# Optimization experiments

Measured on AMD Instinct MI355X. Metric: run time of the kernel, lower is better.

The kernel has to match this reference:

```python
import jax, jax.numpy as jnp
import numpy as np

D_MODEL = 1024
SEL_DIM = 64
CONFIGS = [(4, 32), (8, 64), (16, 128)]  # (heads, dim)
B, T = 2, 2048


def setup_inputs() -> dict:
    key = jax.random.key(0)
    ks = jax.random.split(key, 20)
    s = 0.02  # init scale for stability
    inp = {
        "x": jax.random.normal(ks[0], (B, T, D_MODEL), jnp.float32),
        "sel_w1": jax.random.normal(ks[1], (SEL_DIM, D_MODEL), jnp.float32) * s,
        "sel_b1": jnp.zeros((SEL_DIM,), jnp.float32),
        "sel_w2": jax.random.normal(ks[2], (SEL_DIM, SEL_DIM), jnp.float32) * s,
        "sel_b2": jnp.zeros((SEL_DIM,), jnp.float32),
        "sel_w3": jax.random.normal(ks[3], (len(CONFIGS), SEL_DIM), jnp.float32) * s,
        "sel_b3": jnp.zeros((len(CONFIGS),), jnp.float32),
    }
    for i, (h, d) in enumerate(CONFIGS):
        inp[f"qw{i}"] = jax.random.normal(ks[4 + 3 * i], (h * d, D_MODEL), jnp.float32) * s
        inp[f"kw{i}"] = jax.random.normal(ks[5 + 3 * i], (d, D_MODEL), jnp.float32) * s
        inp[f"ww{i}"] = jax.random.normal(ks[6 + 3 * i], (h, D_MODEL), jnp.float32) * s
    return inp


def _seq_features(x):
    # x: [b,t,d]
    b, t, d = x.shape
    seq_mean = jnp.mean(x, axis=1, keepdims=True)            # [b,1,d]
    seq_std = jnp.std(x, axis=1, keepdims=True, ddof=1)      # torch.std is unbiased
    pos = (jnp.arange(t, dtype=x.dtype) / t)[None, :, None]  # [1,t,1] broadcast to [b,t,d]
    return x + seq_mean + seq_std + pos * 0.1


def _forward(x, sel_w1, sel_b1, sel_w2, sel_b2, sel_w3, sel_b3,
             qw0, kw0, ww0, qw1, kw1, ww1, qw2, kw2, ww2):
    b, t, dm = x.shape
    feats = _seq_features(x)
    h1 = jax.nn.relu(feats @ sel_w1.T + sel_b1)
    h2 = jax.nn.relu(h1 @ sel_w2.T + sel_b2)
    config_probs = jax.nn.softmax(h2 @ sel_w3.T + sel_b3, axis=-1)  # [b,t,ncfg]

    per_cfg = [(qw0, kw0, ww0), (qw1, kw1, ww1), (qw2, kw2, ww2)]
    final = jnp.zeros((b, t, t), dtype=x.dtype)
    for i, ((heads, dim), (qw, kw, ww)) in enumerate(zip(CONFIGS, per_cfg)):
        q = (x @ qw.T).reshape(b, t, heads, dim)   # [b,t,h,d]
        k = x @ kw.T                               # [b,s,d]
        w = x @ ww.T                               # [b,t,h]
        dots = jnp.einsum('bthd,bsd->bths', q, k)  # [b,t,h,s]
        score = jnp.einsum('bths,bth->bts', jax.nn.relu(dots), w)  # relu*weight, sum heads
        final = final + config_probs[:, :, i:i + 1] * score
    return final


def reference(x, sel_w1, sel_b1, sel_w2, sel_b2, sel_w3, sel_b3,
              qw0, kw0, ww0, qw1, kw1, ww1, qw2, kw2, ww2):
    return _forward(x, sel_w1, sel_b1, sel_w2, sel_b2, sel_w3, sel_b3,
                    qw0, kw0, ww0, qw1, kw1, ww1, qw2, kw2, ww2)
```

## Files before the change

kernel.cpp:

```cpp
#include <hip/hip_runtime.h>
#include <cstdint>
#include <cstddef>
#include <math.h>

#define B_ 2
#define T_ 2048
#define D_ 1024
#define M_ (B_*T_)

#define QO0 0
#define KO0 128
#define WO0 160
#define QO1 168
#define KO1 680
#define WO1 744
#define QO2 752
#define KO2 2800
#define WO2 2928
#define SELO 2944
#define LDN 3072

typedef float f32x16 __attribute__((ext_vector_type(16)));
typedef short bf16x8 __attribute__((ext_vector_type(8)));
typedef unsigned short u16;

__device__ __forceinline__ u16 f2bf(float f) {
    unsigned int u = __float_as_uint(f);
    unsigned int r = (u + 0x7fffu + ((u >> 16) & 1u)) >> 16;
    return (u16)r;
}
__device__ __forceinline__ float bf2f(u16 b) {
    return __uint_as_float(((unsigned int)b) << 16);
}

__device__ __forceinline__ void gload16(const void* g, void* l) {
    __builtin_amdgcn_global_load_lds(
        (const __attribute__((address_space(1))) unsigned int*)g,
        (__attribute__((address_space(3))) unsigned int*)l,
        16, 0, 0);
}

__device__ __forceinline__ void stage_plane(const u16* src_base, int row_stride, int k0,
                                            int rg, int lane, u16* dst) {
    int rl  = lane >> 2;
    int row = rg * 16 + rl;
    int q   = (lane & 3) ^ (rl & 3) ^ ((rl >> 2) & 3);
    const u16* s = src_base + (size_t)row * row_stride + k0 + q * 8;
    gload16(s, dst + rg * 512);
}

__global__ void stats_partial(const float* __restrict__ x,
                              float* __restrict__ part, float* __restrict__ part2) {
    int d  = blockIdx.x * 256 + threadIdx.x;
    int tc = blockIdx.y;
    int b  = blockIdx.z;
    const float* p = x + (size_t)b * T_ * D_ + (size_t)tc * 128 * D_ + d;
    float s = 0.f, s2 = 0.f;
    for (int t = 0; t < 128; ++t) {
        float v = p[(size_t)t * D_];
        s += v; s2 += v * v;
    }
    part [(b * 16 + tc) * D_ + d] = s;
    part2[(b * 16 + tc) * D_ + d] = s2;
}

__global__ void stats_final(const float* __restrict__ part, const float* __restrict__ part2,
                            float* __restrict__ ms) {
    int idx = blockIdx.x * 256 + threadIdx.x;
    if (idx >= B_ * D_) return;
    int b = idx / D_, d = idx % D_;
    float s = 0.f, s2 = 0.f;
    for (int i = 0; i < 16; ++i) {
        s  += part [(b * 16 + i) * D_ + d];
        s2 += part2[(b * 16 + i) * D_ + d];
    }
    float mean = s / (float)T_;
    float var  = (s2 - (float)T_ * mean * mean) / (float)(T_ - 1);
    ms[idx] = mean + sqrtf(fmaxf(var, 0.f));
}

__global__ void msdot(const float* __restrict__ ms, const float* __restrict__ w1,
                      float* __restrict__ msd, float* __restrict__ s1) {
    int b = blockIdx.x, j = threadIdx.x;
    const float* wr = w1 + (size_t)j * D_;
    const float* mr = ms + (size_t)b * D_;
    float am = 0.f, as = 0.f;
    for (int d4 = 0; d4 < D_ / 4; ++d4) {
        float4 w = *(const float4*)(wr + d4 * 4);
        float4 m = *(const float4*)(mr + d4 * 4);
        am += w.x * m.x + w.y * m.y + w.z * m.z + w.w * m.w;
        as += w.x + w.y + w.z + w.w;
    }
    msd[b * 64 + j] = am;
    if (b == 0) s1[j] = as;
}

__global__ void split_w(const float* __restrict__ qw0, const float* __restrict__ kw0,
                        const float* __restrict__ ww0, const float* __restrict__ qw1,
                        const float* __restrict__ kw1, const float* __restrict__ ww1,
                        const float* __restrict__ qw2, const float* __restrict__ kw2,
                        const float* __restrict__ ww2, const float* __restrict__ w1s,
                        u16* __restrict__ Wh) {
    int row = blockIdx.x;
    int col = threadIdx.x * 4;
    const float* src = nullptr;
    if      (row < 128)  src = qw0 + (size_t)row * D_;
    else if (row < 160)  src = kw0 + (size_t)(row - 128) * D_;
    else if (row < 164)  src = ww0 + (size_t)(row - 160) * D_;
    else if (row < 168)  src = nullptr;
    else if (row < 680)  src = qw1 + (size_t)(row - 168) * D_;
    else if (row < 744)  src = kw1 + (size_t)(row - 680) * D_;
    else if (row < 752)  src = ww1 + (size_t)(row - 744) * D_;
    else if (row < 2800) src = qw2 + (size_t)(row - 752) * D_;
    else if (row < 2928) src = kw2 + (size_t)(row - 2800) * D_;
    else if (row < 2944) src = ww2 + (size_t)(row - 2928) * D_;
    else if (row < 3008) src = w1s + (size_t)(row - 2944) * D_;
    float4 v = src ? *(const float4*)(src + col) : make_float4(0.f, 0.f, 0.f, 0.f);
    ushort4 h;
    h.x = f2bf(v.x); h.y = f2bf(v.y); h.z = f2bf(v.z); h.w = f2bf(v.w);
    *(ushort4*)&Wh[(size_t)row * D_ + col] = h;
}

__global__ void cast_x(const float* __restrict__ x, u16* __restrict__ Xh) {
    size_t i = ((size_t)blockIdx.x * 256 + threadIdx.x) * 4;
    float4 v = *(const float4*)(x + i);
    ushort4 h;
    h.x = f2bf(v.x); h.y = f2bf(v.y); h.z = f2bf(v.z); h.w = f2bf(v.w);
    *(ushort4*)&Xh[i] = h;
}

__global__ __launch_bounds__(256, 4) void proj_gemm(
    const u16* __restrict__ Xh, const u16* __restrict__ Wh, u16* __restrict__ Ph) {
    __shared__ u16 As[2][4096], Bs[2][4096];
    int tid = threadIdx.x;
    int wave = tid >> 6, lane = tid & 63;
    int bm = blockIdx.x * 128, bn = blockIdx.y * 128;
    int wt = wave >> 1, wn = wave & 1;
    int fm = lane & 31, hv = lane >> 5;
    int tkey = (fm & 3) ^ ((fm >> 2) & 3);
    f32x16 acc[2][2];
#pragma unroll
    for (int i = 0; i < 2; ++i)
#pragma unroll
        for (int j = 0; j < 2; ++j)
#pragma unroll
            for (int r = 0; r < 16; ++r) acc[i][j][r] = 0.f;

    const u16* xh = Xh + (size_t)bm * D_;
    const u16* wh = Wh + (size_t)bn * D_;

    auto stage = [&](int buf, int k0) {
#pragma unroll
        for (int i = 0; i < 4; ++i) {
            int j = wave * 4 + i;
            int pl = j >> 3, rg = j & 7;
            stage_plane(pl ? wh : xh, D_, k0, rg, lane, pl ? Bs[buf] : As[buf]);
        }
    };

    stage(0, 0);
    for (int kc = 0; kc < 32; ++kc) {
        __syncthreads();
        if (kc + 1 < 32) stage((kc + 1) & 1, (kc + 1) * 32);
        const u16* ah = As[kc & 1];
        const u16* bh = Bs[kc & 1];
#pragma unroll
        for (int ks = 0; ks < 2; ++ks) {
            int slot8 = ((ks * 2 + hv) ^ tkey) * 8;
            bf16x8 a_h[2], b_h[2];
#pragma unroll
            for (int t = 0; t < 2; ++t) {
                a_h[t] = *(const bf16x8*)&ah[(wt * 64 + t * 32 + fm) * 32 + slot8];
                b_h[t] = *(const bf16x8*)&bh[(wn * 64 + t * 32 + fm) * 32 + slot8];
            }
#pragma unroll
            for (int ti = 0; ti < 2; ++ti)
#pragma unroll
                for (int tj = 0; tj < 2; ++tj)
                    acc[ti][tj] = __builtin_amdgcn_mfma_f32_32x32x16_bf16(a_h[ti], b_h[tj], acc[ti][tj], 0, 0, 0);
        }
    }
#pragma unroll
    for (int ti = 0; ti < 2; ++ti)
#pragma unroll
        for (int tj = 0; tj < 2; ++tj)
#pragma unroll
            for (int r = 0; r < 16; ++r) {
                int row = bm + wt * 64 + ti * 32 + (r & 3) + 8 * (r >> 2) + 4 * (lane >> 5);
                int col = bn + wn * 64 + tj * 32 + (lane & 31);
                Ph[(size_t)row * LDN + col] = f2bf(acc[ti][tj][r]);
            }
}

__global__ void selector2(const u16* __restrict__ Ph,
                          const float* __restrict__ msd, const float* __restrict__ s1,
                          const float* __restrict__ b1, const float* __restrict__ w2,
                          const float* __restrict__ b2, const float* __restrict__ w3,
                          const float* __restrict__ b3, float* __restrict__ PR) {
    __shared__ float h1s[4][64];
    __shared__ float h2s[4][64];
    __shared__ float lg[4][3];
    int tid = threadIdx.x;
    int slot = tid >> 6, j = tid & 63;
    int bt = blockIdx.x * 4 + slot;
    int b = bt >> 11, t = bt & 2047;
    size_t pidx = (size_t)bt * LDN + SELO + j;
    float v = bf2f(Ph[pidx])
            + msd[b * 64 + j] + 0.1f * ((float)t / (float)T_) * s1[j] + b1[j];
    h1s[slot][j] = fmaxf(v, 0.f);
    __syncthreads();
    float a2 = b2[j];
#pragma unroll 8
    for (int d = 0; d < 64; ++d) a2 = fmaf(h1s[slot][d], w2[j * 64 + d], a2);
    h2s[slot][j] = fmaxf(a2, 0.f);
    __syncthreads();
    if (j < 3) {
        float a3 = b3[j];
        for (int d = 0; d < 64; ++d) a3 = fmaf(h2s[slot][d], w3[j * 64 + d], a3);
        lg[slot][j] = a3;
    }
    __syncthreads();
    if (j == 0) {
        float m = fmaxf(lg[slot][0], fmaxf(lg[slot][1], lg[slot][2]));
        float e0 = expf(lg[slot][0] - m), e1 = expf(lg[slot][1] - m), e2 = expf(lg[slot][2] - m);
        float inv = 1.f / (e0 + e1 + e2);
        PR[bt * 3 + 0] = e0 * inv;
        PR[bt * 3 + 1] = e1 * inv;
        PR[bt * 3 + 2] = e2 * inv;
    }
}

__device__ __forceinline__ int qcol_of(int c) {
    if (c < 2)  return QO0 + c * 64;
    if (c < 10) return QO1 + (c - 2) * 64;
    int u = c - 10;
    return QO2 + (u >> 1) * 128 + (u & 1) * 64;
}

__global__ __launch_bounds__(256, 2) void score_kernel(
    const u16* __restrict__ Ph, const float* __restrict__ PR, float* __restrict__ out) {
    __shared__ u16 Qs[2][8192];
    __shared__ u16 Ks[4 * 4096];
    __shared__ float wpT[28 * 128];
    int tid = threadIdx.x;
    int wave = tid >> 6, lane = tid & 63;
    int wt = wave >> 1, wn = wave & 1;
    int fm = lane & 31, hv = lane >> 5;
    int tkey = (fm & 3) ^ ((fm >> 2) & 3);

    int n = blockIdx.z * 256 + blockIdx.y * 16 + blockIdx.x;
    int p = (n & 7) * 4 + (n >> 7);
    int xb = (n >> 3) & 15;
    int b = p >> 4, yb = p & 15;
    int t0 = yb * 128, s0 = xb * 128;

    const u16* Pq = Ph + (size_t)(b * T_ + t0) * LDN;
    const u16* Pk = Ph + (size_t)(b * T_ + s0) * LDN;

    auto stageQ = [&](int buf, int qcol) {
#pragma unroll
        for (int i = 0; i < 4; ++i) {
            int j = (wave << 2) + i;
            int pl = j >> 3, rg = j & 7;
            stage_plane(Pq, LDN, qcol + pl * 32, rg, lane, &Qs[buf][pl * 4096]);
        }
    };
    auto stageK = [&](int kbase, int nplanes) {
        for (int j = wave; j < nplanes * 8; j += 4) {
            int pl = j >> 3, rg = j & 7;
            stage_plane(Pk, LDN, kbase + pl * 32, rg, lane, &Ks[pl * 4096]);
        }
    };

    stageK(KO0, 1);
    stageQ(0, qcol_of(0));

    for (int idx = tid; idx < 28 * 128; idx += 256) {
        int g = idx >> 7, r = idx & 127;
        int wcol = (g < 4) ? (WO0 + g) : ((g < 12) ? (WO1 + g - 4) : (WO2 + g - 12));
        int cfg  = (g < 4) ? 0 : ((g < 12) ? 1 : 2);
        size_t prow = (size_t)(b * T_ + t0 + r);
        wpT[g * 128 + r] = bf2f(Ph[prow * LDN + wcol]) * PR[prow * 3 + cfg];
    }

    f32x16 outacc[2][2], dots[2][2];
#pragma unroll
    for (int i = 0; i < 2; ++i)
#pragma unroll
        for (int j = 0; j < 2; ++j)
#pragma unroll
            for (int r = 0; r < 16; ++r) { outacc[i][j][r] = 0.f; dots[i][j][r] = 0.f; }

    for (int c = 0; c < 42; ++c) {
        int kp0, kp1, gMid, gEnd;
        if (c < 2)       { kp0 = 0; kp1 = 0; gMid = 2 * c; gEnd = 2 * c + 1; }
        else if (c < 10) { kp0 = 0; kp1 = 1; gMid = -1; gEnd = 4 + (c - 2); }
        else { int u = c - 10; int h = u >> 1, kb = u & 1;
               kp0 = kb * 2; kp1 = kb * 2 + 1; gMid = -1; gEnd = kb ? (12 + h) : -1; }

        __syncthreads();
        if (c < 41) stageQ((c + 1) & 1, qcol_of(c + 1));

        const u16* qb = Qs[c & 1];
#pragma unroll
        for (int ks = 0; ks < 4; ++ks) {
            int slot8 = (((ks & 1) * 2 + hv) ^ tkey) * 8;
            int kp = (ks < 2) ? kp0 : kp1;
            bf16x8 kf[2], qf[2];
#pragma unroll
            for (int tj = 0; tj < 2; ++tj)
                kf[tj] = *(const bf16x8*)&Ks[kp * 4096 + (wn * 64 + tj * 32 + fm) * 32 + slot8];
#pragma unroll
            for (int ti = 0; ti < 2; ++ti)
                qf[ti] = *(const bf16x8*)&qb[(ks >> 1) * 4096 + (wt * 64 + ti * 32 + fm) * 32 + slot8];
#pragma unroll
            for (int ti = 0; ti < 2; ++ti)
#pragma unroll
                for (int tj = 0; tj < 2; ++tj)
                    dots[ti][tj] = __builtin_amdgcn_mfma_f32_32x32x16_bf16(qf[ti], kf[tj], dots[ti][tj], 0, 0, 0);

            int g = (ks == 1) ? gMid : ((ks == 3) ? gEnd : -1);
            if (g >= 0) {
#pragma unroll
                for (int ti = 0; ti < 2; ++ti) {
                    int rowbase = wt * 64 + ti * 32 + 4 * (lane >> 5);
#pragma unroll
                    for (int rq = 0; rq < 4; ++rq) {
                        float4 w4 = *(const float4*)&wpT[g * 128 + rowbase + rq * 8];
                        float wv[4] = {w4.x, w4.y, w4.z, w4.w};
#pragma unroll
                        for (int tj = 0; tj < 2; ++tj)
#pragma unroll
                            for (int r2 = 0; r2 < 4; ++r2) {
                                int r = rq * 4 + r2;
                                outacc[ti][tj][r] += fmaxf(dots[ti][tj][r], 0.f) * wv[r2];
                                dots[ti][tj][r] = 0.f;
                            }
                    }
                }
            }
        }
        if (c == 1)      { __syncthreads(); stageK(KO1, 2); }
        else if (c == 9) { __syncthreads(); stageK(KO2, 4); }
    }

#pragma unroll
    for (int ti = 0; ti < 2; ++ti)
#pragma unroll
        for (int tj = 0; tj < 2; ++tj)
#pragma unroll
            for (int r = 0; r < 16; ++r) {
                int trow = wt * 64 + ti * 32 + (r & 3) + 8 * (r >> 2) + 4 * (lane >> 5);
                int scol = wn * 64 + tj * 32 + (lane & 31);
                out[(size_t)(b * T_ + t0 + trow) * T_ + (s0 + scol)] = outacc[ti][tj][r];
            }
}

extern "C" void kernel_launch(void* const* d_in, const int* in_sizes, int n_in,
                              void* d_out, int out_size, void* d_ws, size_t ws_size,
                              hipStream_t stream) {
    const float* x   = (const float*)d_in[0];
    const float* w1  = (const float*)d_in[1];
    const float* b1  = (const float*)d_in[2];
    const float* w2  = (const float*)d_in[3];
    const float* b2  = (const float*)d_in[4];
    const float* w3  = (const float*)d_in[5];
    const float* b3  = (const float*)d_in[6];
    const float* qw0 = (const float*)d_in[7];
    const float* kw0 = (const float*)d_in[8];
    const float* ww0 = (const float*)d_in[9];
    const float* qw1 = (const float*)d_in[10];
    const float* kw1 = (const float*)d_in[11];
    const float* ww1 = (const float*)d_in[12];
    const float* qw2 = (const float*)d_in[13];
    const float* kw2 = (const float*)d_in[14];
    const float* ww2 = (const float*)d_in[15];
    float* out = (float*)d_out;

    float* fb = (float*)d_ws;
    float* MS  = fb; fb += 2048;
    float* MSD = fb; fb += 128;
    float* S1  = fb; fb += 64;
    float* PR  = fb; fb += (size_t)M_ * 3;
    float* PA  = fb; fb += (size_t)B_ * 16 * D_;
    float* PA2 = fb; fb += (size_t)B_ * 16 * D_;
    u16* ub = (u16*)fb;
    u16* Wh = ub; ub += (size_t)LDN * D_;
    u16* Xh = ub; ub += (size_t)M_ * D_;
    u16* Ph = ub; ub += (size_t)M_ * LDN;

    stats_partial<<<dim3(D_ / 256, 16, B_), 256, 0, stream>>>(x, PA, PA2);
    stats_final<<<dim3((B_ * D_ + 255) / 256), 256, 0, stream>>>(PA, PA2, MS);
    msdot<<<dim3(B_), 64, 0, stream>>>(MS, w1, MSD, S1);
    split_w<<<dim3(LDN), 256, 0, stream>>>(qw0, kw0, ww0, qw1, kw1, ww1,
                                           qw2, kw2, ww2, w1, Wh);
    cast_x<<<dim3((M_ * D_) / 1024), 256, 0, stream>>>(x, Xh);
    proj_gemm<<<dim3(M_ / 128, LDN / 128), 256, 0, stream>>>(Xh, Wh, Ph);
    selector2<<<dim3(M_ / 4), 256, 0, stream>>>(Ph, MSD, S1, b1, w2, b2, w3, b3, PR);
    score_kernel<<<dim3(T_ / 128, T_ / 128, B_), 256, 0, stream>>>(Ph, PR, out);
}
```

Before: 273.5 us.

## Restructure score kernel to 128x64 tiles and fuse stats, cast and selector prep

The x cast is folded into the stats pass, and stats_final is merged with msdot into one kernel. The selector now writes head weights premultiplied by config probabilities as fp16, laid out transposed. The score kernel moves to 128x64 output tiles with a 32-wide K step per iteration, uses less LDS and fewer accumulators, and runs at occupancy 4. The aim is fewer launches, less redundant traffic and better occupancy, at the cost of more loop iterations and fp16 rounding of the weights.

```diff
diff --git a/kernel.cpp b/kernel.cpp
--- a/kernel.cpp
+++ b/kernel.cpp
@@ -1,4 +1,5 @@
 #include <hip/hip_runtime.h>
+#include <hip/hip_fp16.h>
 #include <cstdint>
 #include <cstddef>
 #include <math.h>
@@ -49,50 +50,51 @@
     gload16(s, dst + rg * 512);
 }
 
-__global__ void stats_partial(const float* __restrict__ x,
-                              float* __restrict__ part, float* __restrict__ part2) {
+__global__ void stats1(const float* __restrict__ x, float* __restrict__ part,
+                       float* __restrict__ part2, u16* __restrict__ Xh) {
     int d  = blockIdx.x * 256 + threadIdx.x;
     int tc = blockIdx.y;
     int b  = blockIdx.z;
-    const float* p = x + (size_t)b * T_ * D_ + (size_t)tc * 128 * D_ + d;
+    size_t base = (size_t)b * T_ * D_ + (size_t)tc * 128 * D_ + d;
     float s = 0.f, s2 = 0.f;
     for (int t = 0; t < 128; ++t) {
-        float v = p[(size_t)t * D_];
+        float v = x[base + (size_t)t * D_];
         s += v; s2 += v * v;
+        Xh[base + (size_t)t * D_] = f2bf(v);
     }
     part [(b * 16 + tc) * D_ + d] = s;
     part2[(b * 16 + tc) * D_ + d] = s2;
 }
 
-__global__ void stats_final(const float* __restrict__ part, const float* __restrict__ part2,
-                            float* __restrict__ ms) {
-    int idx = blockIdx.x * 256 + threadIdx.x;
-    if (idx >= B_ * D_) return;
-    int b = idx / D_, d = idx % D_;
+__global__ void stats2(const float* __restrict__ part, const float* __restrict__ part2,
+                       const float* __restrict__ w1,
+                       float* __restrict__ msd, float* __restrict__ s1) {
+    __shared__ float msL[1024];
+    __shared__ float ps[64][17];
+    __shared__ float pw[64][17];
+    int b = blockIdx.x, tid = threadIdx.x;
     float s = 0.f, s2 = 0.f;
     for (int i = 0; i < 16; ++i) {
-        s  += part [(b * 16 + i) * D_ + d];
-        s2 += part2[(b * 16 + i) * D_ + d];
+        s  += part [(b * 16 + i) * D_ + tid];
+        s2 += part2[(b * 16 + i) * D_ + tid];
     }
     float mean = s / (float)T_;
     float var  = (s2 - (float)T_ * mean * mean) / (float)(T_ - 1);
-    ms[idx] = mean + sqrtf(fmaxf(var, 0.f));
-}
-
-__global__ void msdot(const float* __restrict__ ms, const float* __restrict__ w1,
-                      float* __restrict__ msd, float* __restrict__ s1) {
-    int b = blockIdx.x, j = threadIdx.x;
-    const float* wr = w1 + (size_t)j * D_;
-    const float* mr = ms + (size_t)b * D_;
-    float am = 0.f, as = 0.f;
-    for (int d4 = 0; d4 < D_ / 4; ++d4) {
-        float4 w = *(const float4*)(wr + d4 * 4);
-        float4 m = *(const float4*)(mr + d4 * 4);
-        am += w.x * m.x + w.y * m.y + w.z * m.z + w.w * m.w;
-        as += w.x + w.y + w.z + w.w;
-    }
-    msd[b * 64 + j] = am;
-    if (b == 0) s1[j] = as;
+    msL[tid] = mean + sqrtf(fmaxf(var, 0.f));
+    __syncthreads();
+    int j = tid >> 4, cc = tid & 15;
+    float am = 0.f, aw = 0.f;
+    const float* wr = w1 + (size_t)j * D_ + cc * 64;
+    const float* mr = msL + cc * 64;
+    for (int dd = 0; dd < 64; ++dd) { float w = wr[dd]; am += mr[dd] * w; aw += w; }
+    ps[j][cc] = am; pw[j][cc] = aw;
+    __syncthreads();
+    if (tid < 64) {
+        float sm = 0.f, sw = 0.f;
+        for (int i = 0; i < 16; ++i) { sm += ps[tid][i]; sw += pw[tid][i]; }
+        msd[b * 64 + tid] = sm;
+        if (b == 0) s1[tid] = sw;
+    }
 }
 
 __global__ void split_w(const float* __restrict__ qw0, const float* __restrict__ kw0,
@@ -121,14 +123,6 @@
     *(ushort4*)&Wh[(size_t)row * D_ + col] = h;
 }
 
-__global__ void cast_x(const float* __restrict__ x, u16* __restrict__ Xh) {
-    size_t i = ((size_t)blockIdx.x * 256 + threadIdx.x) * 4;
-    float4 v = *(const float4*)(x + i);
-    ushort4 h;
-    h.x = f2bf(v.x); h.y = f2bf(v.y); h.z = f2bf(v.z); h.w = f2bf(v.w);
-    *(ushort4*)&Xh[i] = h;
-}
-
 __global__ __launch_bounds__(256, 4) void proj_gemm(
     const u16* __restrict__ Xh, const u16* __restrict__ Wh, u16* __restrict__ Ph) {
     __shared__ u16 As[2][4096], Bs[2][4096];
@@ -196,7 +190,7 @@
                           const float* __restrict__ msd, const float* __restrict__ s1,
                           const float* __restrict__ b1, const float* __restrict__ w2,
                           const float* __restrict__ b2, const float* __restrict__ w3,
-                          const float* __restrict__ b3, float* __restrict__ PR) {
+                          const float* __restrict__ b3, __half* __restrict__ WP) {
     __shared__ float h1s[4][64];
     __shared__ float h2s[4][64];
     __shared__ float lg[4][3];
@@ -220,140 +214,132 @@
         lg[slot][j] = a3;
     }
     __syncthreads();
-    if (j == 0) {
+    if (j < 28) {
         float m = fmaxf(lg[slot][0], fmaxf(lg[slot][1], lg[slot][2]));
         float e0 = expf(lg[slot][0] - m), e1 = expf(lg[slot][1] - m), e2 = expf(lg[slot][2] - m);
         float inv = 1.f / (e0 + e1 + e2);
-        PR[bt * 3 + 0] = e0 * inv;
-        PR[bt * 3 + 1] = e1 * inv;
-        PR[bt * 3 + 2] = e2 * inv;
-    }
-}
-
-__device__ __forceinline__ int qcol_of(int c) {
-    if (c < 2)  return QO0 + c * 64;
-    if (c < 10) return QO1 + (c - 2) * 64;
-    int u = c - 10;
-    return QO2 + (u >> 1) * 128 + (u & 1) * 64;
-}
-
-__global__ __launch_bounds__(256, 2) void score_kernel(
-    const u16* __restrict__ Ph, const float* __restrict__ PR, float* __restrict__ out) {
-    __shared__ u16 Qs[2][8192];
-    __shared__ u16 Ks[4 * 4096];
-    __shared__ float wpT[28 * 128];
+        int wcol = (j < 4) ? (WO0 + j) : ((j < 12) ? (WO1 + j - 4) : (WO2 + j - 12));
+        float p = ((j < 4) ? e0 : ((j < 12) ? e1 : e2)) * inv;
+        float w = bf2f(Ph[(size_t)bt * LDN + wcol]);
+        WP[(size_t)(b * 28 + j) * T_ + t] = __float2half(w * p);
+    }
+}
+
+__global__ __launch_bounds__(256, 4) void score_kernel(
+    const u16* __restrict__ Ph, const __half* __restrict__ WP, float* __restrict__ out) {
+    __shared__ u16 Qs[2][4096];
+    __shared__ u16 Ks[4][2048];
+    __shared__ __half wpL[3584];
     int tid = threadIdx.x;
     int wave = tid >> 6, lane = tid & 63;
     int wt = wave >> 1, wn = wave & 1;
     int fm = lane & 31, hv = lane >> 5;
     int tkey = (fm & 3) ^ ((fm >> 2) & 3);
 
-    int n = blockIdx.z * 256 + blockIdx.y * 16 + blockIdx.x;
-    int p = (n & 7) * 4 + (n >> 7);
-    int xb = (n >> 3) & 15;
-    int b = p >> 4, yb = p & 15;
-    int t0 = yb * 128, s0 = xb * 128;
+    int n = blockIdx.x;
+    int qt = (n & 7) * 4 + (n >> 8);
+    int b = qt >> 4, t0 = (qt & 15) * 128;
+    int s0 = ((n >> 3) & 31) * 64;
 
     const u16* Pq = Ph + (size_t)(b * T_ + t0) * LDN;
     const u16* Pk = Ph + (size_t)(b * T_ + s0) * LDN;
 
     auto stageQ = [&](int buf, int qcol) {
 #pragma unroll
-        for (int i = 0; i < 4; ++i) {
-            int j = (wave << 2) + i;
-            int pl = j >> 3, rg = j & 7;
-            stage_plane(Pq, LDN, qcol + pl * 32, rg, lane, &Qs[buf][pl * 4096]);
+        for (int i = 0; i < 2; ++i) {
+            int rg = wave * 2 + i;
+            stage_plane(Pq, LDN, qcol, rg, lane, Qs[buf]);
         }
     };
-    auto stageK = [&](int kbase, int nplanes) {
-        for (int j = wave; j < nplanes * 8; j += 4) {
-            int pl = j >> 3, rg = j & 7;
-            stage_plane(Pk, LDN, kbase + pl * 32, rg, lane, &Ks[pl * 4096]);
-        }
-    };
-
-    stageK(KO0, 1);
-    stageQ(0, qcol_of(0));
-
-    for (int idx = tid; idx < 28 * 128; idx += 256) {
-        int g = idx >> 7, r = idx & 127;
-        int wcol = (g < 4) ? (WO0 + g) : ((g < 12) ? (WO1 + g - 4) : (WO2 + g - 12));
-        int cfg  = (g < 4) ? 0 : ((g < 12) ? 1 : 2);
-        size_t prow = (size_t)(b * T_ + t0 + r);
-        wpT[g * 128 + r] = bf2f(Ph[prow * LDN + wcol]) * PR[prow * 3 + cfg];
-    }
-
-    f32x16 outacc[2][2], dots[2][2];
+
+#pragma unroll
+    for (int i = 0; i < 3; ++i) {
+        int j = i * 4 + wave;
+        int pl = j >> 2, rg = j & 3;
+        int col = (pl == 0) ? KO0 : ((pl == 1) ? KO1 : KO1 + 32);
+        stage_plane(Pk, LDN, col, rg, lane, Ks[pl]);
+    }
+#pragma unroll
+    for (int i = 0; i < 2; ++i) {
+        int j = i * 4 + wave;
+        if (j < 7) {
+            const __half* src = WP + (size_t)(b * 28 + j * 4 + (lane >> 4)) * T_ + t0 + (lane & 15) * 8;
+            gload16(src, (u16*)wpL + j * 512);
+        }
+    }
+    stageQ(0, QO0);
+
+    f32x16 outacc[2], dots[2];
 #pragma unroll
     for (int i = 0; i < 2; ++i)
 #pragma unroll
-        for (int j = 0; j < 2; ++j)
-#pragma unroll
-            for (int r = 0; r < 16; ++r) { outacc[i][j][r] = 0.f; dots[i][j][r] = 0.f; }
-
-    for (int c = 0; c < 42; ++c) {
-        int kp0, kp1, gMid, gEnd;
-        if (c < 2)       { kp0 = 0; kp1 = 0; gMid = 2 * c; gEnd = 2 * c + 1; }
-        else if (c < 10) { kp0 = 0; kp1 = 1; gMid = -1; gEnd = 4 + (c - 2); }
-        else { int u = c - 10; int h = u >> 1, kb = u & 1;
-               kp0 = kb * 2; kp1 = kb * 2 + 1; gMid = -1; gEnd = kb ? (12 + h) : -1; }
+        for (int r = 0; r < 16; ++r) { outacc[i][r] = 0.f; dots[i][r] = 0.f; }
+
+    for (int c = 0; c < 84; ++c) {
+        int kp, g;
+        if (c < 4)       { kp = 0; g = c; }
+        else if (c < 20) { int u = c - 4;  kp = 1 + (u & 1); g = (u & 1) ? (4 + (u >> 1)) : -1; }
+        else             { int u = c - 20; kp = u & 3; g = ((u & 3) == 3) ? (12 + (u >> 2)) : -1; }
 
         __syncthreads();
-        if (c < 41) stageQ((c + 1) & 1, qcol_of(c + 1));
+        if (c < 83) {
+            int nc = c + 1;
+            int nq = (nc < 4) ? (QO0 + nc * 32)
+                   : ((nc < 20) ? (QO1 + (nc - 4) * 32) : (QO2 + (nc - 20) * 32));
+            stageQ((nc) & 1, nq);
+        }
 
         const u16* qb = Qs[c & 1];
-#pragma unroll
-        for (int ks = 0; ks < 4; ++ks) {
-            int slot8 = (((ks & 1) * 2 + hv) ^ tkey) * 8;
-            int kp = (ks < 2) ? kp0 : kp1;
-            bf16x8 kf[2], qf[2];
-#pragma unroll
-            for (int tj = 0; tj < 2; ++tj)
-                kf[tj] = *(const bf16x8*)&Ks[kp * 4096 + (wn * 64 + tj * 32 + fm) * 32 + slot8];
-#pragma unroll
-            for (int ti = 0; ti < 2; ++ti)
-                qf[ti] = *(const bf16x8*)&qb[(ks >> 1) * 4096 + (wt * 64 + ti * 32 + fm) * 32 + slot8];
-#pragma unroll
-            for (int ti = 0; ti < 2; ++ti)
-#pragma unroll
-                for (int tj = 0; tj < 2; ++tj)
-                    dots[ti][tj] = __builtin_amdgcn_mfma_f32_32x32x16_bf16(qf[ti], kf[tj], dots[ti][tj], 0, 0, 0);
-
-            int g = (ks == 1) ? gMid : ((ks == 3) ? gEnd : -1);
-            if (g >= 0) {
-#pragma unroll
-                for (int ti = 0; ti < 2; ++ti) {
-                    int rowbase = wt * 64 + ti * 32 + 4 * (lane >> 5);
-#pragma unroll
-                    for (int rq = 0; rq < 4; ++rq) {
-                        float4 w4 = *(const float4*)&wpT[g * 128 + rowbase + rq * 8];
-                        float wv[4] = {w4.x, w4.y, w4.z, w4.w};
-#pragma unroll
-                        for (int tj = 0; tj < 2; ++tj)
-#pragma unroll
-                            for (int r2 = 0; r2 < 4; ++r2) {
-                                int r = rq * 4 + r2;
-                                outacc[ti][tj][r] += fmaxf(dots[ti][tj][r], 0.f) * wv[r2];
-                                dots[ti][tj][r] = 0.f;
-                            }
+        const u16* kb = Ks[kp];
+#pragma unroll
+        for (int ks = 0; ks < 2; ++ks) {
+            int slot8 = ((ks * 2 + hv) ^ tkey) * 8;
+            bf16x8 kf = *(const bf16x8*)&kb[(wn * 32 + fm) * 32 + slot8];
+#pragma unroll
+            for (int ti = 0; ti < 2; ++ti) {
+                bf16x8 qf = *(const bf16x8*)&qb[(wt * 64 + ti * 32 + fm) * 32 + slot8];
+                dots[ti] = __builtin_amdgcn_mfma_f32_32x32x16_bf16(qf, kf, dots[ti], 0, 0, 0);
+            }
+        }
+
+        if (g >= 0) {
+#pragma unroll
+            for (int ti = 0; ti < 2; ++ti) {
+                int rowbase = wt * 64 + ti * 32 + 4 * hv;
+#pragma unroll
+                for (int rq = 0; rq < 4; ++rq) {
+                    const __half2* wp2 = (const __half2*)&wpL[g * 128 + rowbase + rq * 8];
+                    float2 f01 = __half22float2(wp2[0]);
+                    float2 f23 = __half22float2(wp2[1]);
+                    float wv[4] = {f01.x, f01.y, f23.x, f23.y};
+#pragma unroll
+                    for (int r2 = 0; r2 < 4; ++r2) {
+                        int r = rq * 4 + r2;
+                        outacc[ti][r] += fmaxf(dots[ti][r], 0.f) * wv[r2];
+                        dots[ti][r] = 0.f;
                     }
                 }
             }
         }
-        if (c == 1)      { __syncthreads(); stageK(KO1, 2); }
-        else if (c == 9) { __syncthreads(); stageK(KO2, 4); }
+
+        if (c == 19) {
+            __syncthreads();
+#pragma unroll
+            for (int i = 0; i < 4; ++i) {
+                int j = i * 4 + wave;
+                int pl = j >> 2, rg = j & 3;
+                stage_plane(Pk, LDN, KO2 + pl * 32, rg, lane, Ks[pl]);
+            }
+        }
     }
 
 #pragma unroll
     for (int ti = 0; ti < 2; ++ti)
 #pragma unroll
-        for (int tj = 0; tj < 2; ++tj)
-#pragma unroll
-            for (int r = 0; r < 16; ++r) {
-                int trow = wt * 64 + ti * 32 + (r & 3) + 8 * (r >> 2) + 4 * (lane >> 5);
-                int scol = wn * 64 + tj * 32 + (lane & 31);
-                out[(size_t)(b * T_ + t0 + trow) * T_ + (s0 + scol)] = outacc[ti][tj][r];
-            }
+        for (int r = 0; r < 16; ++r) {
+            int row = wt * 64 + ti * 32 + (r & 3) + 8 * (r >> 2) + 4 * hv;
+            out[(size_t)(b * T_ + t0 + row) * T_ + s0 + wn * 32 + fm] = outacc[ti][r];
+        }
 }
 
 extern "C" void kernel_launch(void* const* d_in, const int* in_sizes, int n_in,
@@ -378,24 +364,21 @@
     float* out = (float*)d_out;
 
     float* fb = (float*)d_ws;
-    float* MS  = fb; fb += 2048;
+    float* PA  = fb; fb += (size_t)B_ * 16 * D_;
+    float* PA2 = fb; fb += (size_t)B_ * 16 * D_;
     float* MSD = fb; fb += 128;
     float* S1  = fb; fb += 64;
-    float* PR  = fb; fb += (size_t)M_ * 3;
-    float* PA  = fb; fb += (size_t)B_ * 16 * D_;
-    float* PA2 = fb; fb += (size_t)B_ * 16 * D_;
+    __half* WP = (__half*)fb; fb += (size_t)B_ * 28 * T_ / 2;
     u16* ub = (u16*)fb;
     u16* Wh = ub; ub += (size_t)LDN * D_;
     u16* Xh = ub; ub += (size_t)M_ * D_;
     u16* Ph = ub; ub += (size_t)M_ * LDN;
 
-    stats_partial<<<dim3(D_ / 256, 16, B_), 256, 0, stream>>>(x, PA, PA2);
-    stats_final<<<dim3((B_ * D_ + 255) / 256), 256, 0, stream>>>(PA, PA2, MS);
-    msdot<<<dim3(B_), 64, 0, stream>>>(MS, w1, MSD, S1);
+    stats1<<<dim3(D_ / 256, 16, B_), 256, 0, stream>>>(x, PA, PA2, Xh);
+    stats2<<<dim3(B_), 1024, 0, stream>>>(PA, PA2, w1, MSD, S1);
     split_w<<<dim3(LDN), 256, 0, stream>>>(qw0, kw0, ww0, qw1, kw1, ww1,
                                            qw2, kw2, ww2, w1, Wh);
-    cast_x<<<dim3((M_ * D_) / 1024), 256, 0, stream>>>(x, Xh);
     proj_gemm<<<dim3(M_ / 128, LDN / 128), 256, 0, stream>>>(Xh, Wh, Ph);
-    selector2<<<dim3(M_ / 4), 256, 0, stream>>>(Ph, MSD, S1, b1, w2, b2, w3, b3, PR);
-    score_kernel<<<dim3(T_ / 128, T_ / 128, B_), 256, 0, stream>>>(Ph, PR, out);
-}
+    selector2<<<dim3(M_ / 4), 256, 0, stream>>>(Ph, MSD, S1, b1, w2, b2, w3, b3, WP);
+    score_kernel<<<dim3(1024), 256, 0, stream>>>(Ph, WP, out);
+}
```

After: 269.3 us. Within noise of the previous version (-1.5%).
